# Performance work log

Hardware: AMD Instinct MI355X
Metric: run time of the kernel (lower is better)

Reference implementation:

```python
import jax, jax.numpy as jnp
import numpy as np

N_NODES = 100000
N_EDGES = 1600000
IN_FEATS, HIDDEN, N_CLASSES = 128, 64, 16


def setup_inputs() -> dict:
    key = jax.random.key(0)
    ks = jax.random.split(key, 10)
    feats = jax.random.normal(ks[0], (N_NODES, IN_FEATS), dtype=jnp.float32)
    src = jax.random.randint(ks[1], (N_EDGES,), 0, N_NODES, dtype=jnp.int32)
    dst = jax.random.randint(ks[2], (N_EDGES,), 0, N_NODES, dtype=jnp.int32)
    def glorot(k, fan_in, fan_out):
        lim = np.sqrt(6.0 / (fan_in + fan_out)).astype(np.float32)
        return jax.random.uniform(k, (fan_in, fan_out), jnp.float32, -lim, lim)
    return {
        "features": feats, "src": src, "dst": dst,
        "W0": glorot(ks[3], IN_FEATS, HIDDEN), "b0": jnp.zeros((HIDDEN,), jnp.float32),
        "W1": glorot(ks[4], HIDDEN, HIDDEN), "b1": jnp.zeros((HIDDEN,), jnp.float32),
        "W2": glorot(ks[5], HIDDEN, N_CLASSES), "b2": jnp.zeros((N_CLASSES,), jnp.float32),
    }


def _graph_conv(src, dst, x, W, b, act):
    # DGL GraphConv, norm='both': out = D_in^{-1/2} A (D_out^{-1/2} x) W + b
    n = x.shape[0]
    ones = jnp.ones((src.shape[0],), x.dtype)
    deg_out = jnp.clip(jax.ops.segment_sum(ones, src, num_segments=n), 1.0)
    deg_in = jnp.clip(jax.ops.segment_sum(ones, dst, num_segments=n), 1.0)
    # DGL applies W first when in_dim > out_dim (same math, less edge traffic)
    pre = x.shape[1] > W.shape[1]
    h = x @ W if pre else x
    h = h * jax.lax.rsqrt(deg_out)[:, None]
    agg = jax.ops.segment_sum(h[src], dst, num_segments=n)  # [N, d]
    agg = agg * jax.lax.rsqrt(deg_in)[:, None]
    out = (agg if pre else agg @ W) + b
    return act(out) if act is not None else out


def reference(features, src, dst, W0, b0, W1, b1, W2, b2):
    relu = jax.nn.relu
    h = _graph_conv(src, dst, features, W0, b0, relu)
    h = _graph_conv(src, dst, h, W1, b1, relu)        # dropout p=0.0 -> identity
    h = _graph_conv(src, dst, h, W2, b2, None)
    return h
```

## Files before the change

### kernel.cpp

```cpp
#include <hip/hip_runtime.h>

#define NN 100000
#define NE 1600000
#define NBUCK 782
#define BCAP 2560
#define PCHUNK 8192
#define NPB 196
#define STAGE_CAP 12288

struct alignas(8) US4 { unsigned short x, y, z, w; };

__device__ __forceinline__ float bfu(unsigned int hw) { return __uint_as_float(hw << 16); }
__device__ __forceinline__ unsigned short f2bf(float f) {
    unsigned int u = __float_as_uint(f);
    return (unsigned short)((u + 0x7fffu + ((u >> 16) & 1u)) >> 16);
}


__global__ __launch_bounds__(1024) void k_init(int* __restrict__ cur_d,
                                               int* __restrict__ cur_s,
                                               unsigned short* __restrict__ A,
                                               unsigned short* __restrict__ B,
                                               unsigned short* __restrict__ C16) {
    int t = threadIdx.x;
    for (int b = t; b < NBUCK; b += 1024) {
        cur_d[b] = b * BCAP;
        cur_s[b] = b * BCAP;
    }
    if (t < 64) {
        A[(size_t)NN * 64 + t] = 0;
        B[(size_t)NN * 64 + t] = 0;
    }
    if (t < 16) C16[(size_t)NN * 16 + t] = 0;
}

__global__ __launch_bounds__(512) void k_pairs(const int* __restrict__ src,
                                               const int* __restrict__ dst,
                                               int* __restrict__ cur_d,
                                               int* __restrict__ cur_s,
                                               int* __restrict__ E2d,
                                               unsigned char* __restrict__ E2s) {
    __shared__ int hist[NBUCK], gbase[NBUCK];
    int tid = threadIdx.x;
    int bid = blockIdx.x;
    bool dside = (bid < NPB);
    int chunk = dside ? bid : bid - NPB;
    const int* key = dside ? dst : src;
    int* cur = dside ? cur_d : cur_s;
    for (int i = tid; i < NBUCK; i += 512) hist[i] = 0;
    __syncthreads();
    int base = chunk * PCHUNK;
#pragma unroll
    for (int i = 0; i < PCHUNK / 512; ++i) {
        int e = base + i * 512 + tid;
        if (e < NE) atomicAdd(&hist[key[e] >> 7], 1);
    }
    __syncthreads();
    int rot = (int)((bid * 191u) % NBUCK);
    for (int ii = tid; ii < NBUCK; ii += 512) {
        int i = ii + rot;
        if (i >= NBUCK) i -= NBUCK;
        int h = hist[i];
        if (h) gbase[i] = atomicAdd(&cur[i], h);
        hist[i] = 0;
    }
    __syncthreads();
    if (dside) {
#pragma unroll
        for (int i = 0; i < PCHUNK / 512; ++i) {
            int e = base + i * 512 + tid;
            if (e < NE) {
                int s = src[e], d = dst[e];
                int bd = d >> 7;
                int pd = atomicAdd(&hist[bd], 1);
                E2d[gbase[bd] + pd] = (s << 7) | (d & 127);
            }
        }
    } else {
#pragma unroll
        for (int i = 0; i < PCHUNK / 512; ++i) {
            int e = base + i * 512 + tid;
            if (e < NE) {
                int s = src[e];
                int bs = s >> 7;
                int ps = atomicAdd(&hist[bs], 1);
                E2s[gbase[bs] + ps] = (unsigned char)(s & 127);
            }
        }
    }
}

__global__ __launch_bounds__(256) void k_nodes(int* __restrict__ EB,
                                               const unsigned char* __restrict__ E2s,
                                               const int* __restrict__ cur_d,
                                               const int* __restrict__ cur_s,
                                               int* __restrict__ rowdesc,
                                               float* __restrict__ r_in,
                                               float* __restrict__ r_out) {
    __shared__ int cnt[128], cur[128];
    __shared__ int stage[STAGE_CAP];
    int tid = threadIdx.x;
    int b = blockIdx.x;
    if (b >= NBUCK) {
        b -= NBUCK;
        int base = b * BCAP;
        int end = cur_s[b];
        if (tid < 128) cnt[tid] = 0;
        __syncthreads();
        for (int i = base + tid; i < end; i += 256) atomicAdd(&cnt[E2s[i]], 1);
        __syncthreads();
        if (tid < 128) {
            int node = b * 128 + tid;
            if (node < NN) r_out[node] = rsqrtf((float)max(cnt[tid], 1));
        }
        return;
    }
    int base = b * BCAP;
    int end = cur_d[b];
    int m = min(end - base, STAGE_CAP);
    if (tid < 128) cnt[tid] = 0;
    __syncthreads();
    for (int i = tid; i < m; i += 256) {
        int e = EB[base + i];
        stage[i] = e;
        atomicAdd(&cnt[e & 127], 1);
    }
    __syncthreads();
    int v = (tid < 128) ? cnt[tid] : 0;
    for (int off = 1; off < 128; off <<= 1) {
        int u = (tid >= off && tid < 128) ? cnt[tid - off] : 0;
        __syncthreads();
        if (tid < 128) cnt[tid] += u;
        __syncthreads();
    }
    if (tid < 128) {
        int excl = cnt[tid] - v;
        cur[tid] = excl;
        int node = b * 128 + tid;
        if (node < NN) {
            rowdesc[node] = ((base + excl) << 9) | min(v, 511);
            r_in[node] = rsqrtf((float)max(v, 1));
        }
    }
    __syncthreads();
    for (int i = tid; i < m; i += 256) {
        int e = stage[i];
        int pos = atomicAdd(&cur[e & 127], 1);
        EB[base + pos] = e >> 7;
    }
}


__global__ __launch_bounds__(256) void k_gemm0(const float* __restrict__ x,
                                               const float* __restrict__ W0,
                                               const float* __restrict__ r_out,
                                               unsigned short* __restrict__ A) {
    __shared__ float xl[64 * 129];
    __shared__ float wl[64 * 64];
    int tid = threadIdx.x;
    int m0 = blockIdx.x * 64;
#pragma unroll
    for (int i = 0; i < 8; ++i) {
        int idx = i * 256 + tid;
        int m = idx >> 5, kc = idx & 31;
        int gm = min(m0 + m, NN - 1);
        float4 v = *(const float4*)&x[(size_t)gm * 128 + kc * 4];
        float* p = &xl[m * 129 + kc * 4];
        p[0] = v.x; p[1] = v.y; p[2] = v.z; p[3] = v.w;
    }
    int tn = tid & 15, tm = tid >> 4;
    float acc[4][4] = {};
    const float4* W4 = (const float4*)W0;
    float4* wl4 = (float4*)wl;
    for (int h = 0; h < 2; ++h) {
        __syncthreads();
#pragma unroll
        for (int i = 0; i < 4; ++i) wl4[i * 256 + tid] = W4[h * 1024 + i * 256 + tid];
        __syncthreads();
#pragma unroll 4
        for (int k = 0; k < 64; ++k) {
            int kk = h * 64 + k;
            float4 wv = *(const float4*)&wl[k * 64 + tn * 4];
            float xv[4];
#pragma unroll
            for (int i = 0; i < 4; ++i) xv[i] = xl[(tm * 4 + i) * 129 + kk];
#pragma unroll
            for (int i = 0; i < 4; ++i) {
                acc[i][0] = fmaf(xv[i], wv.x, acc[i][0]);
                acc[i][1] = fmaf(xv[i], wv.y, acc[i][1]);
                acc[i][2] = fmaf(xv[i], wv.z, acc[i][2]);
                acc[i][3] = fmaf(xv[i], wv.w, acc[i][3]);
            }
        }
    }
#pragma unroll
    for (int i = 0; i < 4; ++i) {
        int m = m0 + tm * 4 + i;
        if (m < NN) {
            float ro = r_out[m];
            US4 o = {f2bf(acc[i][0] * ro), f2bf(acc[i][1] * ro),
                     f2bf(acc[i][2] * ro), f2bf(acc[i][3] * ro)};
            *(US4*)&A[(size_t)m * 64 + tn * 4] = o;
        }
    }
}

__global__ __launch_bounds__(256) void k_mlp(const unsigned short* __restrict__ G,
                                             const float* __restrict__ W1,
                                             const float* __restrict__ b1,
                                             const float* __restrict__ W2,
                                             const float* __restrict__ r_out,
                                             unsigned short* __restrict__ C16) {
    __shared__ float gl[64 * 65];
    __shared__ float w1l[64 * 64];
    __shared__ float w2l[64 * 16];
    int tid = threadIdx.x;
    int m0 = blockIdx.x * 64;
#pragma unroll
    for (int i = 0; i < 2; ++i) {
        int idx = i * 256 + tid;
        int m = idx >> 3, c8 = idx & 7;
        int gm = min(m0 + m, NN - 1);
        uint4 u = *(const uint4*)&G[(size_t)gm * 64 + c8 * 8];
        float* p = &gl[m * 65 + c8 * 8];
        p[0] = bfu(u.x & 0xffffu); p[1] = bfu(u.x >> 16);
        p[2] = bfu(u.y & 0xffffu); p[3] = bfu(u.y >> 16);
        p[4] = bfu(u.z & 0xffffu); p[5] = bfu(u.z >> 16);
        p[6] = bfu(u.w & 0xffffu); p[7] = bfu(u.w >> 16);
    }
    float4* w1l4 = (float4*)w1l;
    const float4* W1_4 = (const float4*)W1;
#pragma unroll
    for (int i = 0; i < 4; ++i) w1l4[i * 256 + tid] = W1_4[i * 256 + tid];
    ((float4*)w2l)[tid] = ((const float4*)W2)[tid];
    __syncthreads();
    int tn = tid & 15, tm = tid >> 4;
    float acc[4][4] = {};
#pragma unroll 4
    for (int k = 0; k < 64; ++k) {
        float4 wv = *(const float4*)&w1l[k * 64 + tn * 4];
        float xv[4];
#pragma unroll
        for (int i = 0; i < 4; ++i) xv[i] = gl[(tm * 4 + i) * 65 + k];
#pragma unroll
        for (int i = 0; i < 4; ++i) {
            acc[i][0] = fmaf(xv[i], wv.x, acc[i][0]);
            acc[i][1] = fmaf(xv[i], wv.y, acc[i][1]);
            acc[i][2] = fmaf(xv[i], wv.z, acc[i][2]);
            acc[i][3] = fmaf(xv[i], wv.w, acc[i][3]);
        }
    }
    float4 bb = *(const float4*)&b1[tn * 4];
    __syncthreads();
#pragma unroll
    for (int i = 0; i < 4; ++i) {
        gl[(tm * 4 + i) * 65 + tn * 4 + 0] = fmaxf(acc[i][0] + bb.x, 0.f);
        gl[(tm * 4 + i) * 65 + tn * 4 + 1] = fmaxf(acc[i][1] + bb.y, 0.f);
        gl[(tm * 4 + i) * 65 + tn * 4 + 2] = fmaxf(acc[i][2] + bb.z, 0.f);
        gl[(tm * 4 + i) * 65 + tn * 4 + 3] = fmaxf(acc[i][3] + bb.w, 0.f);
    }
    __syncthreads();
    int m = tid >> 2, n0 = (tid & 3) * 4;
    float a2[4] = {};
#pragma unroll 8
    for (int k = 0; k < 64; ++k) {
        float zv = gl[m * 65 + k];
        float4 wv = *(const float4*)&w2l[k * 16 + n0];
        a2[0] = fmaf(zv, wv.x, a2[0]);
        a2[1] = fmaf(zv, wv.y, a2[1]);
        a2[2] = fmaf(zv, wv.z, a2[2]);
        a2[3] = fmaf(zv, wv.w, a2[3]);
    }
    int node = m0 + m;
    if (node < NN) {
        float ro = r_out[node];
        US4 o = {f2bf(a2[0] * ro), f2bf(a2[1] * ro), f2bf(a2[2] * ro), f2bf(a2[3] * ro)};
        *(US4*)&C16[(size_t)node * 16 + n0] = o;
    }
}


template <int MODE>
__global__ __launch_bounds__(256) void k_gb64(const int* __restrict__ rowdesc,
                                              const int* __restrict__ csr,
                                              const unsigned short* __restrict__ h,
                                              const float* __restrict__ r_in,
                                              const float* __restrict__ r_out,
                                              const float* __restrict__ bias,
                                              unsigned short* __restrict__ o16) {
    int tid = threadIdx.x;
    int wave = tid >> 6, lane = tid & 63;
    int n0 = (blockIdx.x * 4 + wave) * 2, n1 = n0 + 1;
    int rdA = rowdesc[n0], rdB = rowdesc[n1];
    int jbA = rdA >> 9, degA = rdA & 511;
    int jbB = rdB >> 9, degB = rdB & 511;
    int itn = max((degA + 7) >> 3, (degB + 7) >> 3);
    int g = lane >> 3, f8 = lane & 7;
    const int* cA = csr + jbA + g;
    const int* cB = csr + jbB + g;
    const unsigned short* hp = h + f8 * 8;
    float aA[8] = {}, aB[8] = {};
    for (int it = 0; it < itn; it += 2) {
        int s0 = it * 8 + g, s1 = s0 + 8;
        int eA0 = cA[it * 8];
        int eA1 = cA[it * 8 + 8];
        int eB0 = cB[it * 8];
        int eB1 = cB[it * 8 + 8];
        eA0 = (s0 < degA) ? eA0 : NN;
        eA1 = (s1 < degA) ? eA1 : NN;
        eB0 = (s0 < degB) ? eB0 : NN;
        eB1 = (s1 < degB) ? eB1 : NN;
        uint4 u0 = *(const uint4*)(hp + (size_t)eA0 * 64);
        uint4 u1 = *(const uint4*)(hp + (size_t)eA1 * 64);
        uint4 u2 = *(const uint4*)(hp + (size_t)eB0 * 64);
        uint4 u3 = *(const uint4*)(hp + (size_t)eB1 * 64);
        aA[0] += bfu(u0.x & 0xffffu); aA[1] += bfu(u0.x >> 16);
        aA[2] += bfu(u0.y & 0xffffu); aA[3] += bfu(u0.y >> 16);
        aA[4] += bfu(u0.z & 0xffffu); aA[5] += bfu(u0.z >> 16);
        aA[6] += bfu(u0.w & 0xffffu); aA[7] += bfu(u0.w >> 16);
        aA[0] += bfu(u1.x & 0xffffu); aA[1] += bfu(u1.x >> 16);
        aA[2] += bfu(u1.y & 0xffffu); aA[3] += bfu(u1.y >> 16);
        aA[4] += bfu(u1.z & 0xffffu); aA[5] += bfu(u1.z >> 16);
        aA[6] += bfu(u1.w & 0xffffu); aA[7] += bfu(u1.w >> 16);
        aB[0] += bfu(u2.x & 0xffffu); aB[1] += bfu(u2.x >> 16);
        aB[2] += bfu(u2.y & 0xffffu); aB[3] += bfu(u2.y >> 16);
        aB[4] += bfu(u2.z & 0xffffu); aB[5] += bfu(u2.z >> 16);
        aB[6] += bfu(u2.w & 0xffffu); aB[7] += bfu(u2.w >> 16);
        aB[0] += bfu(u3.x & 0xffffu); aB[1] += bfu(u3.x >> 16);
        aB[2] += bfu(u3.y & 0xffffu); aB[3] += bfu(u3.y >> 16);
        aB[4] += bfu(u3.z & 0xffffu); aB[5] += bfu(u3.z >> 16);
        aB[6] += bfu(u3.w & 0xffffu); aB[7] += bfu(u3.w >> 16);
    }
#pragma unroll
    for (int m = 8; m <= 32; m <<= 1) {
#pragma unroll
        for (int k = 0; k < 8; ++k) {
            aA[k] += __shfl_xor(aA[k], m);
            aB[k] += __shfl_xor(aB[k], m);
        }
    }
    if (g < 2) {
        int nw = g ? n1 : n0;
        float o[8];
#pragma unroll
        for (int k = 0; k < 8; ++k) o[k] = g ? aB[k] : aA[k];
        float ri = r_in[nw];
        unsigned short ov[8];
        if (MODE == 0) {
            float ro = r_out[nw];
            float4 bA = *(const float4*)&bias[f8 * 8];
            float4 bB = *(const float4*)&bias[f8 * 8 + 4];
            float bb[8] = {bA.x, bA.y, bA.z, bA.w, bB.x, bB.y, bB.z, bB.w};
#pragma unroll
            for (int k = 0; k < 8; ++k)
                ov[k] = f2bf(fmaxf(fmaf(o[k], ri, bb[k]), 0.f) * ro);
        } else {
#pragma unroll
            for (int k = 0; k < 8; ++k) ov[k] = f2bf(o[k] * ri);
        }
        uint4 ow;
        ow.x = (unsigned)ov[0] | ((unsigned)ov[1] << 16);
        ow.y = (unsigned)ov[2] | ((unsigned)ov[3] << 16);
        ow.z = (unsigned)ov[4] | ((unsigned)ov[5] << 16);
        ow.w = (unsigned)ov[6] | ((unsigned)ov[7] << 16);
        *(uint4*)&o16[(size_t)nw * 64 + f8 * 8] = ow;
    }
}

__global__ __launch_bounds__(256) void k_gb16(const int* __restrict__ rowdesc,
                                              const int* __restrict__ csr,
                                              const unsigned short* __restrict__ C16,
                                              const float* __restrict__ r_in,
                                              const float* __restrict__ b2,
                                              float* __restrict__ out) {
    int tid = threadIdx.x;
    int wave = tid >> 6, lane = tid & 63;
    int n0 = (blockIdx.x * 4 + wave) * 2, n1 = n0 + 1;
    int rdA = rowdesc[n0], rdB = rowdesc[n1];
    int jbA = rdA >> 9, degA = rdA & 511;
    int jbB = rdB >> 9, degB = rdB & 511;
    int itn = max((degA + 7) >> 3, (degB + 7) >> 3);
    int g = lane >> 3, p = lane & 7;
    const int* cA = csr + jbA + g;
    const int* cB = csr + jbB + g;
    const unsigned short* cp = C16 + p * 2;
    float a0A = 0.f, a1A = 0.f, a0B = 0.f, a1B = 0.f;
    for (int it = 0; it < itn; it += 2) {
        int s0 = it * 8 + g, s1 = s0 + 8;
        int eA0 = cA[it * 8];
        int eA1 = cA[it * 8 + 8];
        int eB0 = cB[it * 8];
        int eB1 = cB[it * 8 + 8];
        eA0 = (s0 < degA) ? eA0 : NN;
        eA1 = (s1 < degA) ? eA1 : NN;
        eB0 = (s0 < degB) ? eB0 : NN;
        eB1 = (s1 < degB) ? eB1 : NN;
        unsigned u0 = *(const unsigned*)(cp + (size_t)eA0 * 16);
        unsigned u1 = *(const unsigned*)(cp + (size_t)eA1 * 16);
        unsigned u2 = *(const unsigned*)(cp + (size_t)eB0 * 16);
        unsigned u3 = *(const unsigned*)(cp + (size_t)eB1 * 16);
        a0A += bfu(u0 & 0xffffu); a1A += bfu(u0 >> 16);
        a0A += bfu(u1 & 0xffffu); a1A += bfu(u1 >> 16);
        a0B += bfu(u2 & 0xffffu); a1B += bfu(u2 >> 16);
        a0B += bfu(u3 & 0xffffu); a1B += bfu(u3 >> 16);
    }
#pragma unroll
    for (int m = 8; m <= 32; m <<= 1) {
        a0A += __shfl_xor(a0A, m);
        a1A += __shfl_xor(a1A, m);
        a0B += __shfl_xor(a0B, m);
        a1B += __shfl_xor(a1B, m);
    }
    if (g < 2) {
        int nw = g ? n1 : n0;
        float x0 = g ? a0B : a0A;
        float x1 = g ? a1B : a1A;
        float ri = r_in[nw];
        float2 bb = *(const float2*)&b2[p * 2];
        float2 o;
        o.x = fmaf(x0, ri, bb.x);
        o.y = fmaf(x1, ri, bb.y);
        *(float2*)&out[(size_t)nw * 16 + p * 2] = o;
    }
}

extern "C" void kernel_launch(void* const* d_in, const int* in_sizes, int n_in,
                              void* d_out, int out_size, void* d_ws, size_t ws_size,
                              hipStream_t stream) {
    const float* feats = (const float*)d_in[0];
    const int* src = (const int*)d_in[1];
    const int* dst = (const int*)d_in[2];
    const float* W0 = (const float*)d_in[3];
    const float* b0 = (const float*)d_in[4];
    const float* W1 = (const float*)d_in[5];
    const float* b1 = (const float*)d_in[6];
    const float* W2 = (const float*)d_in[7];
    const float* b2 = (const float*)d_in[8];
    float* out = (float*)d_out;

    float* ws = (float*)d_ws;
    float* r_out = ws;
    float* r_in = ws + NN;
    int* rowdesc = (int*)(ws + 2 * NN);
    int* EB = (int*)(ws + 3 * NN);
    size_t ebw = (size_t)NBUCK * BCAP + 64;
    unsigned char* E2s = (unsigned char*)(ws + 3 * NN + ebw);
    size_t e2sw = ((size_t)NBUCK * BCAP + 3) / 4;
    float* R1 = ws + 3 * NN + ebw + e2sw;
    float* R2 = R1 + (size_t)32 * (NN + 1);
    float* Creg = R2 + (size_t)32 * (NN + 1);
    int* cur_d = (int*)(Creg + (size_t)8 * (NN + 1));
    int* cur_s = cur_d + NBUCK;

    unsigned short* A = (unsigned short*)R1;
    unsigned short* G = A;
    unsigned short* B = (unsigned short*)R2;
    unsigned short* C16 = (unsigned short*)Creg;

    k_init<<<1, 1024, 0, stream>>>(cur_d, cur_s, A, B, C16);
    k_pairs<<<2 * NPB, 512, 0, stream>>>(src, dst, cur_d, cur_s, EB, E2s);
    k_nodes<<<2 * NBUCK, 256, 0, stream>>>(EB, E2s, cur_d, cur_s, rowdesc, r_in, r_out);

    k_gemm0<<<(NN + 63) / 64, 256, 0, stream>>>(feats, W0, r_out, A);
    k_gb64<0><<<NN / 8, 256, 0, stream>>>(rowdesc, EB, A, r_in, r_out, b0, B);

    k_gb64<1><<<NN / 8, 256, 0, stream>>>(rowdesc, EB, B, r_in, r_out, b0, G);
    k_mlp<<<(NN + 63) / 64, 256, 0, stream>>>(G, W1, b1, W2, r_out, C16);

    k_gb16<<<NN / 8, 256, 0, stream>>>(rowdesc, EB, C16, r_in, b2, out);
}
```

Baseline: 278.1 us.

## Replace init kernel with memset, enlarge gemm0 tile, add nontemporal gather loads/stores

Removes the single-block k_init launch: bucket cursors are now zeroed with hipMemsetAsync and the bucket base offset is added at use sites, while the sentinel rows are zeroed inside k_nodes. k_gemm0 now processes 128 rows per block with 8x4 register tiles and stages x in two 64-column halves, halving the block count and raising per-thread reuse of W. The CSR index loads in the gather kernels and their output stores become nontemporal to reduce cache pollution. These are several independent tweaks, and the larger gemm tile uses more registers, which may lower occupancy.

New measurement: 292.2 us. +5.1%, slower.

```diff
diff --git a/kernel.cpp b/kernel.cpp
--- a/kernel.cpp
+++ b/kernel.cpp
@@ -9,6 +9,8 @@
 #define STAGE_CAP 12288
 
 struct alignas(8) US4 { unsigned short x, y, z, w; };
+typedef unsigned int u32x4 __attribute__((ext_vector_type(4)));
+typedef float f32x2 __attribute__((ext_vector_type(2)));
 
 __device__ __forceinline__ float bfu(unsigned int hw) { return __uint_as_float(hw << 16); }
 __device__ __forceinline__ unsigned short f2bf(float f) {
@@ -16,23 +18,6 @@
     return (unsigned short)((u + 0x7fffu + ((u >> 16) & 1u)) >> 16);
 }
 
-
-__global__ __launch_bounds__(1024) void k_init(int* __restrict__ cur_d,
-                                               int* __restrict__ cur_s,
-                                               unsigned short* __restrict__ A,
-                                               unsigned short* __restrict__ B,
-                                               unsigned short* __restrict__ C16) {
-    int t = threadIdx.x;
-    for (int b = t; b < NBUCK; b += 1024) {
-        cur_d[b] = b * BCAP;
-        cur_s[b] = b * BCAP;
-    }
-    if (t < 64) {
-        A[(size_t)NN * 64 + t] = 0;
-        B[(size_t)NN * 64 + t] = 0;
-    }
-    if (t < 16) C16[(size_t)NN * 16 + t] = 0;
-}
 
 __global__ __launch_bounds__(512) void k_pairs(const int* __restrict__ src,
                                                const int* __restrict__ dst,
@@ -73,7 +58,7 @@
                 int s = src[e], d = dst[e];
                 int bd = d >> 7;
                 int pd = atomicAdd(&hist[bd], 1);
-                E2d[gbase[bd] + pd] = (s << 7) | (d & 127);
+                E2d[(size_t)bd * BCAP + gbase[bd] + pd] = (s << 7) | (d & 127);
             }
         }
     } else {
@@ -84,7 +69,7 @@
                 int s = src[e];
                 int bs = s >> 7;
                 int ps = atomicAdd(&hist[bs], 1);
-                E2s[gbase[bs] + ps] = (unsigned char)(s & 127);
+                E2s[(size_t)bs * BCAP + gbase[bs] + ps] = (unsigned char)(s & 127);
             }
         }
     }
@@ -96,15 +81,25 @@
                                                const int* __restrict__ cur_s,
                                                int* __restrict__ rowdesc,
                                                float* __restrict__ r_in,
-                                               float* __restrict__ r_out) {
+                                               float* __restrict__ r_out,
+                                               unsigned short* __restrict__ A,
+                                               unsigned short* __restrict__ B,
+                                               unsigned short* __restrict__ C16) {
     __shared__ int cnt[128], cur[128];
     __shared__ int stage[STAGE_CAP];
     int tid = threadIdx.x;
     int b = blockIdx.x;
+    if (b == 0) {
+        if (tid < 64) {
+            A[(size_t)NN * 64 + tid] = 0;
+            B[(size_t)NN * 64 + tid] = 0;
+        }
+        if (tid < 16) C16[(size_t)NN * 16 + tid] = 0;
+    }
     if (b >= NBUCK) {
         b -= NBUCK;
         int base = b * BCAP;
-        int end = cur_s[b];
+        int end = base + cur_s[b];
         if (tid < 128) cnt[tid] = 0;
         __syncthreads();
         for (int i = base + tid; i < end; i += 256) atomicAdd(&cnt[E2s[i]], 1);
@@ -116,8 +111,7 @@
         return;
     }
     int base = b * BCAP;
-    int end = cur_d[b];
-    int m = min(end - base, STAGE_CAP);
+    int m = min(cur_d[b], STAGE_CAP);
     if (tid < 128) cnt[tid] = 0;
     __syncthreads();
     for (int i = tid; i < m; i += 256) {
@@ -155,37 +149,36 @@
                                                const float* __restrict__ W0,
                                                const float* __restrict__ r_out,
                                                unsigned short* __restrict__ A) {
-    __shared__ float xl[64 * 129];
+    __shared__ float xl[128 * 65];
     __shared__ float wl[64 * 64];
     int tid = threadIdx.x;
-    int m0 = blockIdx.x * 64;
-#pragma unroll
-    for (int i = 0; i < 8; ++i) {
-        int idx = i * 256 + tid;
-        int m = idx >> 5, kc = idx & 31;
-        int gm = min(m0 + m, NN - 1);
-        float4 v = *(const float4*)&x[(size_t)gm * 128 + kc * 4];
-        float* p = &xl[m * 129 + kc * 4];
-        p[0] = v.x; p[1] = v.y; p[2] = v.z; p[3] = v.w;
-    }
+    int m0 = blockIdx.x * 128;
     int tn = tid & 15, tm = tid >> 4;
-    float acc[4][4] = {};
+    float acc[8][4] = {};
     const float4* W4 = (const float4*)W0;
     float4* wl4 = (float4*)wl;
     for (int h = 0; h < 2; ++h) {
         __syncthreads();
 #pragma unroll
+        for (int i = 0; i < 8; ++i) {
+            int idx = i * 256 + tid;
+            int m = idx >> 4, kc = idx & 15;
+            int gm = min(m0 + m, NN - 1);
+            float4 v = *(const float4*)&x[(size_t)gm * 128 + h * 64 + kc * 4];
+            float* p = &xl[m * 65 + kc * 4];
+            p[0] = v.x; p[1] = v.y; p[2] = v.z; p[3] = v.w;
+        }
+#pragma unroll
         for (int i = 0; i < 4; ++i) wl4[i * 256 + tid] = W4[h * 1024 + i * 256 + tid];
         __syncthreads();
 #pragma unroll 4
         for (int k = 0; k < 64; ++k) {
-            int kk = h * 64 + k;
             float4 wv = *(const float4*)&wl[k * 64 + tn * 4];
-            float xv[4];
-#pragma unroll
-            for (int i = 0; i < 4; ++i) xv[i] = xl[(tm * 4 + i) * 129 + kk];
-#pragma unroll
-            for (int i = 0; i < 4; ++i) {
+            float xv[8];
+#pragma unroll
+            for (int i = 0; i < 8; ++i) xv[i] = xl[(tm * 8 + i) * 65 + k];
+#pragma unroll
+            for (int i = 0; i < 8; ++i) {
                 acc[i][0] = fmaf(xv[i], wv.x, acc[i][0]);
                 acc[i][1] = fmaf(xv[i], wv.y, acc[i][1]);
                 acc[i][2] = fmaf(xv[i], wv.z, acc[i][2]);
@@ -194,8 +187,8 @@
         }
     }
 #pragma unroll
-    for (int i = 0; i < 4; ++i) {
-        int m = m0 + tm * 4 + i;
+    for (int i = 0; i < 8; ++i) {
+        int m = m0 + tm * 8 + i;
         if (m < NN) {
             float ro = r_out[m];
             US4 o = {f2bf(acc[i][0] * ro), f2bf(acc[i][1] * ro),
@@ -302,10 +295,10 @@
     float aA[8] = {}, aB[8] = {};
     for (int it = 0; it < itn; it += 2) {
         int s0 = it * 8 + g, s1 = s0 + 8;
-        int eA0 = cA[it * 8];
-        int eA1 = cA[it * 8 + 8];
-        int eB0 = cB[it * 8];
-        int eB1 = cB[it * 8 + 8];
+        int eA0 = __builtin_nontemporal_load(cA + it * 8);
+        int eA1 = __builtin_nontemporal_load(cA + it * 8 + 8);
+        int eB0 = __builtin_nontemporal_load(cB + it * 8);
+        int eB1 = __builtin_nontemporal_load(cB + it * 8 + 8);
         eA0 = (s0 < degA) ? eA0 : NN;
         eA1 = (s1 < degA) ? eA1 : NN;
         eB0 = (s0 < degB) ? eB0 : NN;
@@ -358,12 +351,12 @@
 #pragma unroll
             for (int k = 0; k < 8; ++k) ov[k] = f2bf(o[k] * ri);
         }
-        uint4 ow;
+        u32x4 ow;
         ow.x = (unsigned)ov[0] | ((unsigned)ov[1] << 16);
         ow.y = (unsigned)ov[2] | ((unsigned)ov[3] << 16);
         ow.z = (unsigned)ov[4] | ((unsigned)ov[5] << 16);
         ow.w = (unsigned)ov[6] | ((unsigned)ov[7] << 16);
-        *(uint4*)&o16[(size_t)nw * 64 + f8 * 8] = ow;
+        __builtin_nontemporal_store(ow, (u32x4*)&o16[(size_t)nw * 64 + f8 * 8]);
     }
 }
 
@@ -387,10 +380,10 @@
     float a0A = 0.f, a1A = 0.f, a0B = 0.f, a1B = 0.f;
     for (int it = 0; it < itn; it += 2) {
         int s0 = it * 8 + g, s1 = s0 + 8;
-        int eA0 = cA[it * 8];
-        int eA1 = cA[it * 8 + 8];
-        int eB0 = cB[it * 8];
-        int eB1 = cB[it * 8 + 8];
+        int eA0 = __builtin_nontemporal_load(cA + it * 8);
+        int eA1 = __builtin_nontemporal_load(cA + it * 8 + 8);
+        int eB0 = __builtin_nontemporal_load(cB + it * 8);
+        int eB1 = __builtin_nontemporal_load(cB + it * 8 + 8);
         eA0 = (s0 < degA) ? eA0 : NN;
         eA1 = (s1 < degA) ? eA1 : NN;
         eB0 = (s0 < degB) ? eB0 : NN;
@@ -417,10 +410,10 @@
         float x1 = g ? a1B : a1A;
         float ri = r_in[nw];
         float2 bb = *(const float2*)&b2[p * 2];
-        float2 o;
+        f32x2 o;
         o.x = fmaf(x0, ri, bb.x);
         o.y = fmaf(x1, ri, bb.y);
-        *(float2*)&out[(size_t)nw * 16 + p * 2] = o;
+        __builtin_nontemporal_store(o, (f32x2*)&out[(size_t)nw * 16 + p * 2]);
     }
 }
 
@@ -457,11 +450,12 @@
     unsigned short* B = (unsigned short*)R2;
     unsigned short* C16 = (unsigned short*)Creg;
 
-    k_init<<<1, 1024, 0, stream>>>(cur_d, cur_s, A, B, C16);
+    hipMemsetAsync(cur_d, 0, 2 * NBUCK * sizeof(int), stream);
     k_pairs<<<2 * NPB, 512, 0, stream>>>(src, dst, cur_d, cur_s, EB, E2s);
-    k_nodes<<<2 * NBUCK, 256, 0, stream>>>(EB, E2s, cur_d, cur_s, rowdesc, r_in, r_out);
-
-    k_gemm0<<<(NN + 63) / 64, 256, 0, stream>>>(feats, W0, r_out, A);
+    k_nodes<<<2 * NBUCK, 256, 0, stream>>>(EB, E2s, cur_d, cur_s, rowdesc, r_in, r_out,
+                                           A, B, C16);
+
+    k_gemm0<<<(NN + 127) / 128, 256, 0, stream>>>(feats, W0, r_out, A);
     k_gb64<0><<<NN / 8, 256, 0, stream>>>(rowdesc, EB, A, r_in, r_out, b0, B);
 
     k_gb64<1><<<NN / 8, 256, 0, stream>>>(rowdesc, EB, B, r_in, r_out, b0, G);
```
